# Kernel tuning notes

Hardware: AMD Instinct MI355X
Metric: run time of the kernel (lower is better)

Reference implementation:

```python
import jax, jax.numpy as jnp
import numpy as np

N_NODES = 50000
N_EDGES = 800000
FEATS = 128
HIDDEN = 64
CLASSES = 64


def graph_conv(x, edges):
    """GCN-style symmetric-normalized aggregation over an edge list (no self-loops;
    self information is supplied via the concat in the host module)."""
    src, dst = edges[0], edges[1]
    ones = jnp.ones((edges.shape[1],), dtype=x.dtype)
    deg = jax.ops.segment_sum(ones, dst, num_segments=N_NODES)
    inv_sqrt = jax.lax.rsqrt(jnp.maximum(deg, 1.0))
    coef = inv_sqrt[src] * inv_sqrt[dst]            # [E]
    msg = x[src] * coef[:, None]                     # [E, H] gather
    return jax.ops.segment_sum(msg, dst, num_segments=N_NODES)  # [N, H] scatter


def setup_inputs() -> dict:
    key = jax.random.key(0)
    ks = jax.random.split(key, 16)
    def lin(k, out_d, in_d):
        return jax.random.normal(k, (out_d, in_d), dtype=jnp.float32) / np.sqrt(in_d)
    x = jax.random.normal(ks[0], (N_NODES, FEATS), dtype=jnp.float32)
    edges = jax.random.randint(ks[1], (2, N_EDGES), 0, N_NODES, dtype=jnp.int64)
    return {
        "x": x,
        "edges": edges,
        "W1": lin(ks[2], HIDDEN, FEATS),
        "b1": jnp.zeros((HIDDEN,), dtype=jnp.float32),
        "W2": lin(ks[3], HIDDEN, 2 * HIDDEN),
        "A2a": lin(ks[4], HIDDEN, HIDDEN),
        "A2b": lin(ks[5], HIDDEN, HIDDEN),
        "W3": lin(ks[6], HIDDEN, 2 * HIDDEN),
        "A3a": lin(ks[7], HIDDEN, HIDDEN),
        "A3b": lin(ks[8], HIDDEN, HIDDEN),
        "W4": lin(ks[9], CLASSES, 2 * HIDDEN),
        "A4a": lin(ks[10], CLASSES, HIDDEN),
        "A4b": lin(ks[11], CLASSES, HIDDEN),
    }


def _block(x, edges, W, Aa, Ab):
    # relu(Linear(cat[x, conv(x)]) + att_a(x) * att_b(x))
    h = graph_conv(x, edges)
    cat = jnp.concatenate([x, h], axis=1)            # [N, 2H]
    return jax.nn.relu(cat @ W.T + (x @ Aa.T) * (x @ Ab.T))


def reference(x, edges, W1, b1, W2, A2a, A2b, W3, A3a, A3b, W4, A4a, A4b):
    x = jax.nn.relu(x @ W1.T + b1)                   # [N, H]
    x = _block(x, edges, W2, A2a, A2b)               # [N, H]
    x = _block(x, edges, W3, A3a, A3b)               # [N, H]
    x = _block(x, edges, W4, A4a, A4b)               # [N, C]
    return x
```

## Files before the change

### kernel.cpp

```cpp
#include <hip/hip_runtime.h>
#include <hip/hip_bf16.h>
#include <hip/hip_fp16.h>

#define N_NODES 50000
#define N_EDGES 800000
#define NTILES 3125
#define W_TOTAL 57344
#define WB2 192
#define CLS_UNITS 1024
#define CLS_STRIDE (128 * 256)
#define CLS_RANGE 6250
#define TB 782
#define ROWCAP 64

typedef __attribute__((ext_vector_type(8))) short bf16x8;
typedef __attribute__((ext_vector_type(4))) float f32x4;
typedef __attribute__((ext_vector_type(8))) unsigned short u16x8;

__device__ inline unsigned short f2bf(float f) {
    unsigned int x = __float_as_uint(f);
    unsigned int r = (x + 0x7FFF + ((x >> 16) & 1)) >> 16;
    return (unsigned short)r;
}
__device__ inline float2 h2f2(unsigned int u) {
    __half2 h = *(__half2*)&u;
    return make_float2(__low2float(h), __high2float(h));
}
__device__ inline unsigned int f22h2(float a, float b) {
    __half2 h = __floats2half2_rn(a, b);
    return *(unsigned int*)&h;
}

__global__ __launch_bounds__(256) void pass1_kernel(
    const float* __restrict__ x, const int* __restrict__ src, const int* __restrict__ dst,
    const float* __restrict__ W1, const float* __restrict__ b1,
    const float* W2, const float* A2a, const float* A2b,
    const float* W3, const float* A3a, const float* A3b,
    const float* W4, const float* A4a, const float* A4b,
    int* __restrict__ cnt, unsigned short* __restrict__ srcAp,
    unsigned short* __restrict__ wp, __half* __restrict__ Ht) {
    int tid = threadIdx.x;

    if (blockIdx.x < CLS_UNITS) {
        int cls = blockIdx.x & 7;
        int k = blockIdx.x >> 3;
        int lo = cls * CLS_RANGE, hi = lo + CLS_RANGE;
        for (int e = k * 256 + tid; e < N_EDGES; e += CLS_STRIDE) {
            int d = dst[e];
            if (d >= lo && d < hi) {
                int pos = atomicAdd(&cnt[d], 1);
                if (pos < ROWCAP) srcAp[(size_t)d * ROWCAP + pos] = (unsigned short)src[e];
            }
        }
        return;
    }
    if (blockIdx.x >= CLS_UNITS + TB) {
        int i = 8192 + (blockIdx.x - CLS_UNITS - TB) * 256 + tid;
        if (i >= W_TOTAL) return;
        float v;
        if (i < 16384)      v = W2[i - 8192];
        else if (i < 20480) v = A2a[i - 16384];
        else if (i < 24576) v = A2b[i - 20480];
        else if (i < 32768) v = W3[i - 24576];
        else if (i < 36864) v = A3a[i - 32768];
        else if (i < 40960) v = A3b[i - 36864];
        else if (i < 49152) v = W4[i - 40960];
        else if (i < 53248) v = A4a[i - 49152];
        else                v = A4b[i - 53248];
        wp[i] = f2bf(v);
        return;
    }

    int wave = ((blockIdx.x - CLS_UNITS) * 256 + tid) >> 6;
    if (wave >= NTILES) return;
    int lane = tid & 63;
    int r16 = lane & 15, quad = lane >> 4;
    int base = wave * 16;

    bf16x8 a[4];
    const float* xr = x + (size_t)(base + r16) * 128 + quad * 8;
#pragma unroll
    for (int kb = 0; kb < 4; kb++) {
        float4 f0 = *(const float4*)(xr + kb * 32);
        float4 f1 = *(const float4*)(xr + kb * 32 + 4);
        bf16x8 v;
        v[0] = (short)f2bf(f0.x); v[1] = (short)f2bf(f0.y);
        v[2] = (short)f2bf(f0.z); v[3] = (short)f2bf(f0.w);
        v[4] = (short)f2bf(f1.x); v[5] = (short)f2bf(f1.y);
        v[6] = (short)f2bf(f1.z); v[7] = (short)f2bf(f1.w);
        a[kb] = v;
    }

#pragma unroll
    for (int jt = 0; jt < 4; jt++) {
        f32x4 acc = {0.f, 0.f, 0.f, 0.f};
        const float* wr = W1 + (size_t)(jt * 16 + r16) * 128 + quad * 8;
#pragma unroll
        for (int kb = 0; kb < 4; kb++) {
            float4 g0 = *(const float4*)(wr + kb * 32);
            float4 g1 = *(const float4*)(wr + kb * 32 + 4);
            bf16x8 b;
            b[0] = (short)f2bf(g0.x); b[1] = (short)f2bf(g0.y);
            b[2] = (short)f2bf(g0.z); b[3] = (short)f2bf(g0.w);
            b[4] = (short)f2bf(g1.x); b[5] = (short)f2bf(g1.y);
            b[6] = (short)f2bf(g1.z); b[7] = (short)f2bf(g1.w);
            acc = __builtin_amdgcn_mfma_f32_16x16x32_bf16(a[kb], b, acc, 0, 0, 0);
        }
        int col = jt * 16 + r16;
        float bias = b1[col];
#pragma unroll
        for (int r = 0; r < 4; r++) {
            int row = base + quad * 4 + r;
            float v = fmaxf(acc[r] + bias, 0.f);
            Ht[(size_t)row * 64 + col] = __float2half(v);
        }
    }
}

__global__ __launch_bounds__(256) void scale_kernel(const int* __restrict__ cnt,
                                                    const __half* __restrict__ Ht,
                                                    __half* __restrict__ As,
                                                    float* __restrict__ isq,
                                                    float* __restrict__ sdeg) {
    int t = blockIdx.x * 256 + threadIdx.x;
    int row = t >> 4, sl = t & 15;
    if (row >= N_NODES) return;
    float dv = fmaxf((float)cnt[row], 1.0f);
    float is = rsqrtf(dv);
    if (sl == 0) {
        isq[row] = is;
        sdeg[row] = sqrtf(dv);
    }
    uint2 rv = *((const uint2*)(Ht + (size_t)row * 64) + sl);
    float2 fa = h2f2(rv.x), fb = h2f2(rv.y);
    uint2 ov;
    ov.x = f22h2(fa.x * is, fa.y * is);
    ov.y = f22h2(fb.x * is, fb.y * is);
    *((uint2*)(As + (size_t)row * 64) + sl) = ov;
}

__global__ __launch_bounds__(256) void conv_dense_k(const __half* __restrict__ hs,
                                                    const int* __restrict__ cnt,
                                                    const unsigned short* __restrict__ srcAp,
                                                    const float* __restrict__ isq,
                                                    const float* __restrict__ sdeg,
                                                    const unsigned short* __restrict__ wp,
                                                    const unsigned short* __restrict__ aap,
                                                    const unsigned short* __restrict__ abp,
                                                    __half* __restrict__ outs,
                                                    float* __restrict__ outf,
                                                    int finalLayer) {
    __shared__ unsigned short clds[64][64];
    int tid = threadIdx.x;
    int wv = tid >> 6;
    int lane = tid & 63;
    int t = blockIdx.x * 4 + wv;
    if (t >= NTILES) return;
    int base = t * 16;

    {
        int e8 = lane >> 3, fl = lane & 7;
        const unsigned int* hsp = (const unsigned int*)hs;
#pragma unroll
        for (int g = 0; g < 2; g++) {
            int lrow = g * 8 + e8;
            int row = base + lrow;
            int b = row * ROWCAP;
            int cv = min(cnt[row], ROWCAP);
            float acc[8];
#pragma unroll
            for (int k = 0; k < 8; k++) acc[k] = 0.f;
            for (int i = 0; i < cv; i += 4) {
#pragma unroll
                for (int u = 0; u < 4; u++) {
                    int j = i + u;
                    bool ok = j < cv;
                    int s = srcAp[b + j];
                    s = ok ? s : 0;
                    uint4 raw = *(const uint4*)(hsp + (size_t)s * 32 + fl * 4);
                    unsigned int msk = ok ? 0xFFFFFFFFu : 0u;
                    float2 f0 = h2f2(raw.x & msk);
                    float2 f1 = h2f2(raw.y & msk);
                    float2 f2 = h2f2(raw.z & msk);
                    float2 f3 = h2f2(raw.w & msk);
                    acc[0] += f0.x; acc[1] += f0.y; acc[2] += f1.x; acc[3] += f1.y;
                    acc[4] += f2.x; acc[5] += f2.y; acc[6] += f3.x; acc[7] += f3.y;
                }
            }
            float sc = isq[row];
            u16x8 o;
#pragma unroll
            for (int k = 0; k < 8; k++) o[k] = f2bf(acc[k] * sc);
            *(u16x8*)(&clds[wv * 16 + lrow][fl * 8]) = o;
        }
    }

    int r16 = lane & 15, quad = lane >> 4;
    float rs = sdeg[base + r16];
    const unsigned int* hr = (const unsigned int*)(hs + (size_t)(base + r16) * 64) + quad * 4;
    uint4 raw0 = *(const uint4*)(hr);
    uint4 raw1 = *(const uint4*)(hr + 16);
    bf16x8 ha0, ha1;
    {
        float2 f;
        f = h2f2(raw0.x); ha0[0] = (short)f2bf(f.x * rs); ha0[1] = (short)f2bf(f.y * rs);
        f = h2f2(raw0.y); ha0[2] = (short)f2bf(f.x * rs); ha0[3] = (short)f2bf(f.y * rs);
        f = h2f2(raw0.z); ha0[4] = (short)f2bf(f.x * rs); ha0[5] = (short)f2bf(f.y * rs);
        f = h2f2(raw0.w); ha0[6] = (short)f2bf(f.x * rs); ha0[7] = (short)f2bf(f.y * rs);
        f = h2f2(raw1.x); ha1[0] = (short)f2bf(f.x * rs); ha1[1] = (short)f2bf(f.y * rs);
        f = h2f2(raw1.y); ha1[2] = (short)f2bf(f.x * rs); ha1[3] = (short)f2bf(f.y * rs);
        f = h2f2(raw1.z); ha1[4] = (short)f2bf(f.x * rs); ha1[5] = (short)f2bf(f.y * rs);
        f = h2f2(raw1.w); ha1[6] = (short)f2bf(f.x * rs); ha1[7] = (short)f2bf(f.y * rs);
    }
    bf16x8 ca0 = *(const bf16x8*)(&clds[wv * 16 + r16][quad * 8]);
    bf16x8 ca1 = *(const bf16x8*)(&clds[wv * 16 + r16][32 + quad * 8]);

    float isq4[4];
    if (!finalLayer) {
#pragma unroll
        for (int r = 0; r < 4; r++) isq4[r] = isq[base + quad * 4 + r];
    }

#pragma unroll
    for (int jt = 0; jt < 4; jt++) {
        const unsigned short* wr = wp + (size_t)(jt * 16 + r16) * 128 + quad * 8;
        const unsigned short* ar = aap + (size_t)(jt * 16 + r16) * 64 + quad * 8;
        const unsigned short* br = abp + (size_t)(jt * 16 + r16) * 64 + quad * 8;
        f32x4 P = {0.f, 0.f, 0.f, 0.f};
        f32x4 Q = {0.f, 0.f, 0.f, 0.f};
        f32x4 R = {0.f, 0.f, 0.f, 0.f};
        P = __builtin_amdgcn_mfma_f32_16x16x32_bf16(ha0, *(const bf16x8*)(wr), P, 0, 0, 0);
        P = __builtin_amdgcn_mfma_f32_16x16x32_bf16(ha1, *(const bf16x8*)(wr + 32), P, 0, 0, 0);
        P = __builtin_amdgcn_mfma_f32_16x16x32_bf16(ca0, *(const bf16x8*)(wr + 64), P, 0, 0, 0);
        P = __builtin_amdgcn_mfma_f32_16x16x32_bf16(ca1, *(const bf16x8*)(wr + 96), P, 0, 0, 0);
        Q = __builtin_amdgcn_mfma_f32_16x16x32_bf16(ha0, *(const bf16x8*)(ar), Q, 0, 0, 0);
        Q = __builtin_amdgcn_mfma_f32_16x16x32_bf16(ha1, *(const bf16x8*)(ar + 32), Q, 0, 0, 0);
        R = __builtin_amdgcn_mfma_f32_16x16x32_bf16(ha0, *(const bf16x8*)(br), R, 0, 0, 0);
        R = __builtin_amdgcn_mfma_f32_16x16x32_bf16(ha1, *(const bf16x8*)(br + 32), R, 0, 0, 0);
        int col = jt * 16 + r16;
#pragma unroll
        for (int r = 0; r < 4; r++) {
            int row = base + quad * 4 + r;
            float v = fmaxf(P[r] + Q[r] * R[r], 0.f);
            if (finalLayer) outf[(size_t)row * 64 + col] = v;
            else            outs[(size_t)row * 64 + col] = __float2half(v * isq4[r]);
        }
    }
}

extern "C" void kernel_launch(void* const* d_in, const int* in_sizes, int n_in,
                              void* d_out, int out_size, void* d_ws, size_t ws_size,
                              hipStream_t stream) {
    const float* x = (const float*)d_in[0];
    const int* edges = (const int*)d_in[1];
    const float* W1 = (const float*)d_in[2];
    const float* b1 = (const float*)d_in[3];
    const float* W2 = (const float*)d_in[4];
    const float* A2a = (const float*)d_in[5];
    const float* A2b = (const float*)d_in[6];
    const float* W3 = (const float*)d_in[7];
    const float* A3a = (const float*)d_in[8];
    const float* A3b = (const float*)d_in[9];
    const float* W4 = (const float*)d_in[10];
    const float* A4a = (const float*)d_in[11];
    const float* A4b = (const float*)d_in[12];
    float* out = (float*)d_out;

    const int* src = edges;
    const int* dst = edges + N_EDGES;

    char* p = (char*)d_ws;
    auto alloc = [&](size_t bytes) {
        char* r = p;
        p += (bytes + 255) & ~(size_t)255;
        return r;
    };
    int* cnt              = (int*)alloc(N_NODES * 4);
    float* isq            = (float*)alloc(N_NODES * 4);
    float* sdeg           = (float*)alloc(N_NODES * 4);
    unsigned short* srcAp = (unsigned short*)alloc((size_t)N_NODES * ROWCAP * 2);
    unsigned short* wpAll = (unsigned short*)alloc(W_TOTAL * 2);
    __half* Ht            = (__half*)alloc((size_t)N_NODES * 64 * 2);
    __half* As            = (__half*)alloc((size_t)N_NODES * 64 * 2);
    __half* Bs            = (__half*)alloc((size_t)N_NODES * 64 * 2);

    const unsigned short* W2p  = wpAll + 8192;
    const unsigned short* A2ap = wpAll + 16384;
    const unsigned short* A2bp = wpAll + 20480;
    const unsigned short* W3p  = wpAll + 24576;
    const unsigned short* A3ap = wpAll + 32768;
    const unsigned short* A3bp = wpAll + 36864;
    const unsigned short* W4p  = wpAll + 40960;
    const unsigned short* A4ap = wpAll + 49152;
    const unsigned short* A4bp = wpAll + 53248;

    hipMemsetAsync(cnt, 0, N_NODES * 4, stream);
    pass1_kernel<<<CLS_UNITS + TB + WB2, 256, 0, stream>>>(
        x, src, dst, W1, b1, W2, A2a, A2b, W3, A3a, A3b, W4, A4a, A4b,
        cnt, srcAp, wpAll, Ht);

    scale_kernel<<<(N_NODES * 16 + 255) / 256, 256, 0, stream>>>(cnt, Ht, As, isq, sdeg);

    conv_dense_k<<<TB, 256, 0, stream>>>(As, cnt, srcAp, isq, sdeg,
                                         W2p, A2ap, A2bp, Bs, nullptr, 0);
    conv_dense_k<<<TB, 256, 0, stream>>>(Bs, cnt, srcAp, isq, sdeg,
                                         W3p, A3ap, A3bp, As, nullptr, 0);
    conv_dense_k<<<TB, 256, 0, stream>>>(As, cnt, srcAp, isq, sdeg,
                                         W4p, A4ap, A4bp, nullptr, out, 1);
}
```

Measured before the change: 232.1 us.

## Switch MFMA path to fp16 and drop scale pre-pass with per-edge scaling

Replaces the bf16 conversion and MFMA path with native fp16 (_Float16) MFMA, removing the manual bf16 rounding code and the fp16-to-bf16 repacking of the self features. Replaces the scale kernel, which wrote a prescaled copy of the first hidden layer, with a tiny isq kernel. The first conv layer now applies the source inv-sqrt-degree per edge by gathering isq[s]. The gather loop is unrolled 8-wide and uses FMA with a zero weight instead of masking loads, and sdeg is stored as half. This saves one full pass over node features at the cost of an extra scattered isq load per edge in layer 1, and it changes numerics to fp16.

```diff
diff --git a/kernel.cpp b/kernel.cpp
--- a/kernel.cpp
+++ b/kernel.cpp
@@ -12,23 +12,16 @@
 #define CLS_RANGE 6250
 #define TB 782
 #define ROWCAP 64
-
-typedef __attribute__((ext_vector_type(8))) short bf16x8;
+#define ISQ_NB 196
+
+typedef __attribute__((ext_vector_type(8))) _Float16 h16x8;
+typedef __attribute__((ext_vector_type(2))) _Float16 h16x2;
 typedef __attribute__((ext_vector_type(4))) float f32x4;
-typedef __attribute__((ext_vector_type(8))) unsigned short u16x8;
-
-__device__ inline unsigned short f2bf(float f) {
-    unsigned int x = __float_as_uint(f);
-    unsigned int r = (x + 0x7FFF + ((x >> 16) & 1)) >> 16;
-    return (unsigned short)r;
-}
+
 __device__ inline float2 h2f2(unsigned int u) {
-    __half2 h = *(__half2*)&u;
-    return make_float2(__low2float(h), __high2float(h));
-}
-__device__ inline unsigned int f22h2(float a, float b) {
-    __half2 h = __floats2half2_rn(a, b);
-    return *(unsigned int*)&h;
+    union { unsigned int u32; h16x2 h; } cv;
+    cv.u32 = u;
+    return make_float2((float)cv.h.x, (float)cv.h.y);
 }
 
 __global__ __launch_bounds__(256) void pass1_kernel(
@@ -38,7 +31,7 @@
     const float* W3, const float* A3a, const float* A3b,
     const float* W4, const float* A4a, const float* A4b,
     int* __restrict__ cnt, unsigned short* __restrict__ srcAp,
-    unsigned short* __restrict__ wp, __half* __restrict__ Ht) {
+    _Float16* __restrict__ wp, _Float16* __restrict__ Ht) {
     int tid = threadIdx.x;
 
     if (blockIdx.x < CLS_UNITS) {
@@ -67,7 +60,7 @@
         else if (i < 49152) v = W4[i - 40960];
         else if (i < 53248) v = A4a[i - 49152];
         else                v = A4b[i - 53248];
-        wp[i] = f2bf(v);
+        wp[i] = (_Float16)v;
         return;
     }
 
@@ -77,17 +70,17 @@
     int r16 = lane & 15, quad = lane >> 4;
     int base = wave * 16;
 
-    bf16x8 a[4];
+    h16x8 a[4];
     const float* xr = x + (size_t)(base + r16) * 128 + quad * 8;
 #pragma unroll
     for (int kb = 0; kb < 4; kb++) {
         float4 f0 = *(const float4*)(xr + kb * 32);
         float4 f1 = *(const float4*)(xr + kb * 32 + 4);
-        bf16x8 v;
-        v[0] = (short)f2bf(f0.x); v[1] = (short)f2bf(f0.y);
-        v[2] = (short)f2bf(f0.z); v[3] = (short)f2bf(f0.w);
-        v[4] = (short)f2bf(f1.x); v[5] = (short)f2bf(f1.y);
-        v[6] = (short)f2bf(f1.z); v[7] = (short)f2bf(f1.w);
+        h16x8 v;
+        v[0] = (_Float16)f0.x; v[1] = (_Float16)f0.y;
+        v[2] = (_Float16)f0.z; v[3] = (_Float16)f0.w;
+        v[4] = (_Float16)f1.x; v[5] = (_Float16)f1.y;
+        v[6] = (_Float16)f1.z; v[7] = (_Float16)f1.w;
         a[kb] = v;
     }
 
@@ -99,12 +92,12 @@
         for (int kb = 0; kb < 4; kb++) {
             float4 g0 = *(const float4*)(wr + kb * 32);
             float4 g1 = *(const float4*)(wr + kb * 32 + 4);
-            bf16x8 b;
-            b[0] = (short)f2bf(g0.x); b[1] = (short)f2bf(g0.y);
-            b[2] = (short)f2bf(g0.z); b[3] = (short)f2bf(g0.w);
-            b[4] = (short)f2bf(g1.x); b[5] = (short)f2bf(g1.y);
-            b[6] = (short)f2bf(g1.z); b[7] = (short)f2bf(g1.w);
-            acc = __builtin_amdgcn_mfma_f32_16x16x32_bf16(a[kb], b, acc, 0, 0, 0);
+            h16x8 b;
+            b[0] = (_Float16)g0.x; b[1] = (_Float16)g0.y;
+            b[2] = (_Float16)g0.z; b[3] = (_Float16)g0.w;
+            b[4] = (_Float16)g1.x; b[5] = (_Float16)g1.y;
+            b[6] = (_Float16)g1.z; b[7] = (_Float16)g1.w;
+            acc = __builtin_amdgcn_mfma_f32_16x16x32_f16(a[kb], b, acc, 0, 0, 0);
         }
         int col = jt * 16 + r16;
         float bias = b1[col];
@@ -112,45 +105,34 @@
         for (int r = 0; r < 4; r++) {
             int row = base + quad * 4 + r;
             float v = fmaxf(acc[r] + bias, 0.f);
-            Ht[(size_t)row * 64 + col] = __float2half(v);
-        }
-    }
-}
-
-__global__ __launch_bounds__(256) void scale_kernel(const int* __restrict__ cnt,
-                                                    const __half* __restrict__ Ht,
-                                                    __half* __restrict__ As,
-                                                    float* __restrict__ isq,
-                                                    float* __restrict__ sdeg) {
-    int t = blockIdx.x * 256 + threadIdx.x;
-    int row = t >> 4, sl = t & 15;
-    if (row >= N_NODES) return;
-    float dv = fmaxf((float)cnt[row], 1.0f);
-    float is = rsqrtf(dv);
-    if (sl == 0) {
-        isq[row] = is;
-        sdeg[row] = sqrtf(dv);
-    }
-    uint2 rv = *((const uint2*)(Ht + (size_t)row * 64) + sl);
-    float2 fa = h2f2(rv.x), fb = h2f2(rv.y);
-    uint2 ov;
-    ov.x = f22h2(fa.x * is, fa.y * is);
-    ov.y = f22h2(fb.x * is, fb.y * is);
-    *((uint2*)(As + (size_t)row * 64) + sl) = ov;
-}
-
-__global__ __launch_bounds__(256) void conv_dense_k(const __half* __restrict__ hs,
+            Ht[(size_t)row * 64 + col] = (_Float16)v;
+        }
+    }
+}
+
+__global__ __launch_bounds__(256) void isq_kernel(const int* __restrict__ cnt,
+                                                  float* __restrict__ isq,
+                                                  _Float16* __restrict__ sdeg) {
+    int i = blockIdx.x * 256 + threadIdx.x;
+    if (i >= N_NODES) return;
+    float dv = fmaxf((float)cnt[i], 1.0f);
+    isq[i] = rsqrtf(dv);
+    sdeg[i] = (_Float16)sqrtf(dv);
+}
+
+__global__ __launch_bounds__(256) void conv_dense_k(const _Float16* __restrict__ hs,
                                                     const int* __restrict__ cnt,
                                                     const unsigned short* __restrict__ srcAp,
                                                     const float* __restrict__ isq,
-                                                    const float* __restrict__ sdeg,
-                                                    const unsigned short* __restrict__ wp,
-                                                    const unsigned short* __restrict__ aap,
-                                                    const unsigned short* __restrict__ abp,
-                                                    __half* __restrict__ outs,
+                                                    const _Float16* __restrict__ sdeg,
+                                                    const _Float16* __restrict__ wp,
+                                                    const _Float16* __restrict__ aap,
+                                                    const _Float16* __restrict__ abp,
+                                                    _Float16* __restrict__ outs,
                                                     float* __restrict__ outf,
+                                                    int perEdgeScale,
                                                     int finalLayer) {
-    __shared__ unsigned short clds[64][64];
+    __shared__ _Float16 clds[64][64];
     int tid = threadIdx.x;
     int wv = tid >> 6;
     int lane = tid & 63;
@@ -166,54 +148,45 @@
             int lrow = g * 8 + e8;
             int row = base + lrow;
             int b = row * ROWCAP;
-            int cv = min(cnt[row], ROWCAP);
+            int cntv = cnt[row];
+            int cv = min(cntv, ROWCAP);
             float acc[8];
 #pragma unroll
             for (int k = 0; k < 8; k++) acc[k] = 0.f;
-            for (int i = 0; i < cv; i += 4) {
-#pragma unroll
-                for (int u = 0; u < 4; u++) {
+            for (int i = 0; i < cv; i += 8) {
+#pragma unroll
+                for (int u = 0; u < 8; u++) {
                     int j = i + u;
                     bool ok = j < cv;
                     int s = srcAp[b + j];
-                    s = ok ? s : 0;
                     uint4 raw = *(const uint4*)(hsp + (size_t)s * 32 + fl * 4);
-                    unsigned int msk = ok ? 0xFFFFFFFFu : 0u;
-                    float2 f0 = h2f2(raw.x & msk);
-                    float2 f1 = h2f2(raw.y & msk);
-                    float2 f2 = h2f2(raw.z & msk);
-                    float2 f3 = h2f2(raw.w & msk);
-                    acc[0] += f0.x; acc[1] += f0.y; acc[2] += f1.x; acc[3] += f1.y;
-                    acc[4] += f2.x; acc[5] += f2.y; acc[6] += f3.x; acc[7] += f3.y;
+                    float w;
+                    if (perEdgeScale) w = ok ? isq[s] : 0.f;
+                    else              w = ok ? 1.f : 0.f;
+                    float2 f0 = h2f2(raw.x), f1 = h2f2(raw.y);
+                    float2 f2 = h2f2(raw.z), f3 = h2f2(raw.w);
+                    acc[0] = fmaf(f0.x, w, acc[0]); acc[1] = fmaf(f0.y, w, acc[1]);
+                    acc[2] = fmaf(f1.x, w, acc[2]); acc[3] = fmaf(f1.y, w, acc[3]);
+                    acc[4] = fmaf(f2.x, w, acc[4]); acc[5] = fmaf(f2.y, w, acc[5]);
+                    acc[6] = fmaf(f3.x, w, acc[6]); acc[7] = fmaf(f3.y, w, acc[7]);
                 }
             }
-            float sc = isq[row];
-            u16x8 o;
-#pragma unroll
-            for (int k = 0; k < 8; k++) o[k] = f2bf(acc[k] * sc);
-            *(u16x8*)(&clds[wv * 16 + lrow][fl * 8]) = o;
+            float sc = rsqrtf(fmaxf((float)cntv, 1.0f));
+            h16x8 o;
+#pragma unroll
+            for (int k = 0; k < 8; k++) o[k] = (_Float16)(acc[k] * sc);
+            *(h16x8*)(&clds[lrow + wv * 16][fl * 8]) = o;
         }
     }
 
     int r16 = lane & 15, quad = lane >> 4;
-    float rs = sdeg[base + r16];
-    const unsigned int* hr = (const unsigned int*)(hs + (size_t)(base + r16) * 64) + quad * 4;
-    uint4 raw0 = *(const uint4*)(hr);
-    uint4 raw1 = *(const uint4*)(hr + 16);
-    bf16x8 ha0, ha1;
-    {
-        float2 f;
-        f = h2f2(raw0.x); ha0[0] = (short)f2bf(f.x * rs); ha0[1] = (short)f2bf(f.y * rs);
-        f = h2f2(raw0.y); ha0[2] = (short)f2bf(f.x * rs); ha0[3] = (short)f2bf(f.y * rs);
-        f = h2f2(raw0.z); ha0[4] = (short)f2bf(f.x * rs); ha0[5] = (short)f2bf(f.y * rs);
-        f = h2f2(raw0.w); ha0[6] = (short)f2bf(f.x * rs); ha0[7] = (short)f2bf(f.y * rs);
-        f = h2f2(raw1.x); ha1[0] = (short)f2bf(f.x * rs); ha1[1] = (short)f2bf(f.y * rs);
-        f = h2f2(raw1.y); ha1[2] = (short)f2bf(f.x * rs); ha1[3] = (short)f2bf(f.y * rs);
-        f = h2f2(raw1.z); ha1[4] = (short)f2bf(f.x * rs); ha1[5] = (short)f2bf(f.y * rs);
-        f = h2f2(raw1.w); ha1[6] = (short)f2bf(f.x * rs); ha1[7] = (short)f2bf(f.y * rs);
-    }
-    bf16x8 ca0 = *(const bf16x8*)(&clds[wv * 16 + r16][quad * 8]);
-    bf16x8 ca1 = *(const bf16x8*)(&clds[wv * 16 + r16][32 + quad * 8]);
+    _Float16 rs = finalLayer || !perEdgeScale ? sdeg[base + r16] : (_Float16)1.0f;
+    if (perEdgeScale) rs = (_Float16)1.0f;
+    const _Float16* hr = hs + (size_t)(base + r16) * 64 + quad * 8;
+    h16x8 ha0 = *(const h16x8*)(hr) * rs;
+    h16x8 ha1 = *(const h16x8*)(hr + 32) * rs;
+    h16x8 ca0 = *(const h16x8*)(&clds[wv * 16 + r16][quad * 8]);
+    h16x8 ca1 = *(const h16x8*)(&clds[wv * 16 + r16][32 + quad * 8]);
 
     float isq4[4];
     if (!finalLayer) {
@@ -223,27 +196,27 @@
 
 #pragma unroll
     for (int jt = 0; jt < 4; jt++) {
-        const unsigned short* wr = wp + (size_t)(jt * 16 + r16) * 128 + quad * 8;
-        const unsigned short* ar = aap + (size_t)(jt * 16 + r16) * 64 + quad * 8;
-        const unsigned short* br = abp + (size_t)(jt * 16 + r16) * 64 + quad * 8;
+        const _Float16* wr = wp + (size_t)(jt * 16 + r16) * 128 + quad * 8;
+        const _Float16* ar = aap + (size_t)(jt * 16 + r16) * 64 + quad * 8;
+        const _Float16* br = abp + (size_t)(jt * 16 + r16) * 64 + quad * 8;
         f32x4 P = {0.f, 0.f, 0.f, 0.f};
         f32x4 Q = {0.f, 0.f, 0.f, 0.f};
         f32x4 R = {0.f, 0.f, 0.f, 0.f};
-        P = __builtin_amdgcn_mfma_f32_16x16x32_bf16(ha0, *(const bf16x8*)(wr), P, 0, 0, 0);
-        P = __builtin_amdgcn_mfma_f32_16x16x32_bf16(ha1, *(const bf16x8*)(wr + 32), P, 0, 0, 0);
-        P = __builtin_amdgcn_mfma_f32_16x16x32_bf16(ca0, *(const bf16x8*)(wr + 64), P, 0, 0, 0);
-        P = __builtin_amdgcn_mfma_f32_16x16x32_bf16(ca1, *(const bf16x8*)(wr + 96), P, 0, 0, 0);
-        Q = __builtin_amdgcn_mfma_f32_16x16x32_bf16(ha0, *(const bf16x8*)(ar), Q, 0, 0, 0);
-        Q = __builtin_amdgcn_mfma_f32_16x16x32_bf16(ha1, *(const bf16x8*)(ar + 32), Q, 0, 0, 0);
-        R = __builtin_amdgcn_mfma_f32_16x16x32_bf16(ha0, *(const bf16x8*)(br), R, 0, 0, 0);
-        R = __builtin_amdgcn_mfma_f32_16x16x32_bf16(ha1, *(const bf16x8*)(br + 32), R, 0, 0, 0);
+        P = __builtin_amdgcn_mfma_f32_16x16x32_f16(ha0, *(const h16x8*)(wr), P, 0, 0, 0);
+        P = __builtin_amdgcn_mfma_f32_16x16x32_f16(ha1, *(const h16x8*)(wr + 32), P, 0, 0, 0);
+        P = __builtin_amdgcn_mfma_f32_16x16x32_f16(ca0, *(const h16x8*)(wr + 64), P, 0, 0, 0);
+        P = __builtin_amdgcn_mfma_f32_16x16x32_f16(ca1, *(const h16x8*)(wr + 96), P, 0, 0, 0);
+        Q = __builtin_amdgcn_mfma_f32_16x16x32_f16(ha0, *(const h16x8*)(ar), Q, 0, 0, 0);
+        Q = __builtin_amdgcn_mfma_f32_16x16x32_f16(ha1, *(const h16x8*)(ar + 32), Q, 0, 0, 0);
+        R = __builtin_amdgcn_mfma_f32_16x16x32_f16(ha0, *(const h16x8*)(br), R, 0, 0, 0);
+        R = __builtin_amdgcn_mfma_f32_16x16x32_f16(ha1, *(const h16x8*)(br + 32), R, 0, 0, 0);
         int col = jt * 16 + r16;
 #pragma unroll
         for (int r = 0; r < 4; r++) {
             int row = base + quad * 4 + r;
             float v = fmaxf(P[r] + Q[r] * R[r], 0.f);
             if (finalLayer) outf[(size_t)row * 64 + col] = v;
-            else            outs[(size_t)row * 64 + col] = __float2half(v * isq4[r]);
+            else            outs[(size_t)row * 64 + col] = (_Float16)(v * isq4[r]);
         }
     }
 }
@@ -277,34 +250,34 @@
     };
     int* cnt              = (int*)alloc(N_NODES * 4);
     float* isq            = (float*)alloc(N_NODES * 4);
-    float* sdeg           = (float*)alloc(N_NODES * 4);
+    _Float16* sdeg        = (_Float16*)alloc(N_NODES * 2);
     unsigned short* srcAp = (unsigned short*)alloc((size_t)N_NODES * ROWCAP * 2);
-    unsigned short* wpAll = (unsigned short*)alloc(W_TOTAL * 2);
-    __half* Ht            = (__half*)alloc((size_t)N_NODES * 64 * 2);
-    __half* As            = (__half*)alloc((size_t)N_NODES * 64 * 2);
-    __half* Bs            = (__half*)alloc((size_t)N_NODES * 64 * 2);
-
-    const unsigned short* W2p  = wpAll + 8192;
-    const unsigned short* A2ap = wpAll + 16384;
-    const unsigned short* A2bp = wpAll + 20480;
-    const unsigned short* W3p  = wpAll + 24576;
-    const unsigned short* A3ap = wpAll + 32768;
-    const unsigned short* A3bp = wpAll + 36864;
-    const unsigned short* W4p  = wpAll + 40960;
-    const unsigned short* A4ap = wpAll + 49152;
-    const unsigned short* A4bp = wpAll + 53248;
+    _Float16* wpAll       = (_Float16*)alloc(W_TOTAL * 2);
+    _Float16* Ht          = (_Float16*)alloc((size_t)N_NODES * 64 * 2);
+    _Float16* Bs          = (_Float16*)alloc((size_t)N_NODES * 64 * 2);
+    _Float16* As          = (_Float16*)alloc((size_t)N_NODES * 64 * 2);
+
+    const _Float16* W2p  = wpAll + 8192;
+    const _Float16* A2ap = wpAll + 16384;
+    const _Float16* A2bp = wpAll + 20480;
+    const _Float16* W3p  = wpAll + 24576;
+    const _Float16* A3ap = wpAll + 32768;
+    const _Float16* A3bp = wpAll + 36864;
+    const _Float16* W4p  = wpAll + 40960;
+    const _Float16* A4ap = wpAll + 49152;
+    const _Float16* A4bp = wpAll + 53248;
 
     hipMemsetAsync(cnt, 0, N_NODES * 4, stream);
     pass1_kernel<<<CLS_UNITS + TB + WB2, 256, 0, stream>>>(
         x, src, dst, W1, b1, W2, A2a, A2b, W3, A3a, A3b, W4, A4a, A4b,
         cnt, srcAp, wpAll, Ht);
 
-    scale_kernel<<<(N_NODES * 16 + 255) / 256, 256, 0, stream>>>(cnt, Ht, As, isq, sdeg);
-
+    isq_kernel<<<ISQ_NB, 256, 0, stream>>>(cnt, isq, sdeg);
+
+    conv_dense_k<<<TB, 256, 0, stream>>>(Ht, cnt, srcAp, isq, sdeg,
+                                         W2p, A2ap, A2bp, Bs, nullptr, 1, 0);
+    conv_dense_k<<<TB, 256, 0, stream>>>(Bs, cnt, srcAp, isq, sdeg,
+                                         W3p, A3ap, A3bp, As, nullptr, 0, 0);
     conv_dense_k<<<TB, 256, 0, stream>>>(As, cnt, srcAp, isq, sdeg,
-                                         W2p, A2ap, A2bp, Bs, nullptr, 0);
-    conv_dense_k<<<TB, 256, 0, stream>>>(Bs, cnt, srcAp, isq, sdeg,
-                                         W3p, A3ap, A3bp, As, nullptr, 0);
-    conv_dense_k<<<TB, 256, 0, stream>>>(As, cnt, srcAp, isq, sdeg,
-                                         W4p, A4ap, A4bp, nullptr, out, 1);
-}
+                                         W4p, A4ap, A4bp, nullptr, out, 0, 1);
+}
```

After: 282.9 us. 21.9% more time.
